# Kernel tuning notes

Measured on AMD Instinct MI355X. Metric: run time of the kernel, lower is better.

The kernel has to match this reference:

```python
import jax, jax.numpy as jnp
import numpy as np
from jax import lax

G, K, C_IN, C_FEAT, H, W, B = 8, 6, 512, 256, 64, 64, 1


def apply_offset(offset):
    # offset: [N, 2, H, W] pixel-space offsets -> sampling grid [N, H, W, 2] in [-1, 1]
    # channel 0 displaces x (width), channel 1 displaces y (height), matching the
    # reversed-meshgrid logic of the original torch apply_offset.
    n, _, h, w = offset.shape
    jj = jnp.arange(w, dtype=offset.dtype)[None, None, :]
    ii = jnp.arange(h, dtype=offset.dtype)[None, :, None]
    gx = (jj + offset[:, 0]) / ((w - 1.0) / 2.0) - 1.0
    gy = (ii + offset[:, 1]) / ((h - 1.0) / 2.0) - 1.0
    return jnp.stack([gx, gy], axis=-1)


def grid_sample_border(img, grid):
    # img: [N, C, H, W], grid: [N, H, W, 2] in [-1, 1]
    # Bilinear, padding_mode='border', align_corners=False (torch grid_sample default).
    n, c, h, w = img.shape
    x = jnp.clip((grid[..., 0] + 1.0) * w * 0.5 - 0.5, 0.0, w - 1.0)
    y = jnp.clip((grid[..., 1] + 1.0) * h * 0.5 - 0.5, 0.0, h - 1.0)
    x0 = jnp.floor(x)
    y0 = jnp.floor(y)
    wx = (x - x0)[:, None]  # [N,1,H,W]
    wy = (y - y0)[:, None]
    x0i = x0.astype(jnp.int32)
    y0i = y0.astype(jnp.int32)
    x1i = jnp.minimum(x0i + 1, w - 1)
    y1i = jnp.minimum(y0i + 1, h - 1)

    def gather(im, yi, xi):  # im [C,H,W]; yi, xi [H,W]
        return im[:, yi, xi]

    g = jax.vmap(gather)
    v00 = g(img, y0i, x0i)
    v01 = g(img, y0i, x1i)
    v10 = g(img, y1i, x0i)
    v11 = g(img, y1i, x1i)
    return (1.0 - wy) * ((1.0 - wx) * v00 + wx * v01) + wy * ((1.0 - wx) * v10 + wx * v11)


def setup_inputs() -> dict:
    key = jax.random.key(0)
    ks = jax.random.split(key, 11)
    s = 0.02
    return {
        "gar_feat": jax.random.normal(ks[0], (B, C_FEAT, H, W), jnp.float32),
        "cond_feat": jax.random.normal(ks[1], (B, C_FEAT, H, W), jnp.float32),
        "mask": jax.random.uniform(ks[2], (B, G, C_FEAT), dtype=jnp.float32),
        "W1": jax.random.normal(ks[3], (G, 128, C_IN, 3, 3), jnp.float32) * s,
        "b1": jax.random.normal(ks[4], (G, 128), jnp.float32) * s,
        "W2": jax.random.normal(ks[5], (G, 64, 128, 3, 3), jnp.float32) * s,
        "b2": jax.random.normal(ks[6], (G, 64), jnp.float32) * s,
        "W3": jax.random.normal(ks[7], (G, 32, 64, 3, 3), jnp.float32) * s,
        "b3": jax.random.normal(ks[8], (G, 32), jnp.float32) * s,
        "W4": jax.random.normal(ks[9], (G, 3 * K, 32, 3, 3), jnp.float32) * s,
        "b4": jax.random.normal(ks[10], (G, 3 * K), jnp.float32) * s,
    }


def reference(gar_feat, cond_feat, mask, W1, b1, W2, b2, W3, b3, W4, b4):
    b, c, h, w = gar_feat.shape
    g = W1.shape[0]
    k = W4.shape[1] // 3
    inp = jnp.concatenate([gar_feat, cond_feat], axis=1)  # [B, 2C, H, W]

    def conv(x, wgt, bias):
        return lax.conv_general_dilated(
            x, wgt, (1, 1), 'SAME', dimension_numbers=('NCHW', 'OIHW', 'NCHW')
        ) + bias[None, :, None, None]

    def lrelu(x):
        return jnp.where(x >= 0, x, 0.1 * x)

    def group_net(w1, bb1, w2, bb2, w3, bb3, w4, bb4):
        hid = lrelu(conv(inp, w1, bb1))
        hid = lrelu(conv(hid, w2, bb2))
        hid = lrelu(conv(hid, w3, bb3))
        return conv(hid, w4, bb4)  # [B, 3k, H, W]

    oa = jax.vmap(group_net)(W1, b1, W2, b2, W3, b3, W4, b4)  # [G, B, 3k, H, W]
    attn = jax.nn.softmax(oa[:, :, 2 * k:], axis=0)           # softmax across groups: [G,B,k,H,W]
    off = oa[:, :, :2 * k].reshape(g, b * k, 2, h, w)
    grid = jax.vmap(apply_offset)(off)                        # [G, B*k, H, W, 2]

    rep = jnp.repeat(gar_feat, k, axis=0)                     # [B*k, C, H, W]

    def warp_group(grid_g, attn_g, mask_g):
        samp = grid_sample_border(rep, grid_g).reshape(b, k, c, h, w)
        wfeat = jnp.sum(samp * attn_g[:, :, None], axis=1)    # [B, C, H, W]
        return wfeat * mask_g[:, :, None, None]

    warped = jax.vmap(warp_group)(grid, attn, jnp.transpose(mask, (1, 0, 2)))
    return jnp.sum(warped, axis=0)  # [B, C, H, W]
```

## Files before the change

kernel.cpp:

```cpp
#include <hip/hip_runtime.h>
#include <hip/hip_bf16.h>

typedef __hip_bfloat16 bf16;
typedef unsigned short ushort8v __attribute__((ext_vector_type(8)));
typedef short  s16x4  __attribute__((ext_vector_type(4)));
typedef short  bf16x8 __attribute__((ext_vector_type(8)));
typedef float  f32x4  __attribute__((ext_vector_type(4)));

#define HW 4096
#define IMG_W 64

__device__ __forceinline__ float bfbits2f(unsigned short u) {
    return __uint_as_float(((unsigned int)u) << 16);
}
__device__ __forceinline__ short f2bs(float f) {
    bf16 h = __float2bfloat16(f);
    return *reinterpret_cast<short*>(&h);
}

__device__ __forceinline__ void gl_lds16(const void* g, void* s) {
    __builtin_amdgcn_global_load_lds(
        (const __attribute__((address_space(1))) unsigned int*)g,
        (__attribute__((address_space(3))) unsigned int*)s, 16, 0, 0);
}

__device__ void pack_input_dev(const float* __restrict__ gar,
                               const float* __restrict__ cond,
                               short* __restrict__ outp,
                               short* __restrict__ gart, int bx2, float* tile)
{
    int bx = bx2 & 127;
    int by = bx2 >> 7;
    int tx = threadIdx.x & 31;
    int ty = threadIdx.x >> 5;
#pragma unroll
    for (int i = 0; i < 4; ++i) {
        int c = by * 32 + ty + i * 8;
        const float* src = (c < 256) ? (gar + (size_t)c * HW)
                                     : (cond + (size_t)(c - 256) * HW);
        tile[(ty + i * 8) * 33 + tx] = src[bx * 32 + tx];
    }
    __syncthreads();
#pragma unroll
    for (int i = 0; i < 4; ++i) {
        int p = bx * 32 + ty + i * 8;
        short v = f2bs(tile[tx * 33 + ty + i * 8]);
        outp[((size_t)by * 4096 + p) * 32 + tx] = v;
        if (by < 8)
            gart[(size_t)p * 256 + by * 32 + tx] = v;
    }
}

template<int CIN, int CREAL, int BN, int NT, bool COAL>
__device__ void pack_w_dev(const float* __restrict__ wgt, char* __restrict__ wp,
                           int bx, short* sT)
{
    constexpr int NCC  = CIN / 32;
    constexpr int BLKB = 9 * 4 * BN * 16;

    const int t  = threadIdx.x;
    const int cc = bx % NCC;
    const int nt = (bx / NCC) % NT;
    const int g  = bx / (NT * NCC);

    for (int i = t; i < BLKB / 8; i += 256)
        reinterpret_cast<s16x4*>(sT)[i] = s16x4{0, 0, 0, 0};
    __syncthreads();

    int ocmax = CREAL - nt * BN; if (ocmax > BN) ocmax = BN;
    const size_t base = ((size_t)(g * CREAL + nt * BN) * CIN + cc * 32) * 9;
    for (int i = t; i < ocmax * 288; i += 256) {
        int oc = i / 288;
        int r  = i % 288;
        int ic = r / 9, tap = r % 9;
        size_t idx;
        if (COAL) idx = (size_t)(((tap * BN + oc) * 4 + (ic >> 3)) * 8 + (ic & 7));
        else      idx = (size_t)(((tap * 4 + (ic >> 3)) * BN + oc) * 8 + (ic & 7));
        sT[idx] = f2bs(wgt[base + (size_t)oc * CIN * 9 + r]);
    }
    __syncthreads();

    const s16x4* src = reinterpret_cast<const s16x4*>(sT);
    s16x4* dst = reinterpret_cast<s16x4*>(wp + (size_t)bx * BLKB);
    for (int i = t; i < BLKB / 8; i += 256)
        dst[i] = src[i];
}

__global__ __launch_bounds__(256)
void pack_all(const float* __restrict__ gar, const float* __restrict__ cond,
              const float* __restrict__ W1, const float* __restrict__ W2,
              const float* __restrict__ W3, const float* __restrict__ W4,
              short* inp_t, short* gar_t,
              char* W1p, char* W2p, char* W3p, char* W4p)
{
    __shared__ __align__(16) short sbuf[9 * 4 * 64 * 8];
    int bx = blockIdx.x;
    if (bx < 256)      pack_w_dev<512, 128, 64, 2, true>(W1, W1p, bx,       sbuf);
    else if (bx < 288) pack_w_dev<128,  64, 64, 1, true>(W2, W2p, bx - 256, sbuf);
    else if (bx < 304) pack_w_dev< 64,  32, 32, 1, true>(W3, W3p, bx - 288, sbuf);
    else if (bx < 312) pack_w_dev< 32,  18, 32, 1, true>(W4, W4p, bx - 304, sbuf);
    else pack_input_dev(gar, cond, inp_t, gar_t, bx - 312, (float*)sbuf);
}

__global__ __launch_bounds__(256, 2)
void conv1_p2(const short* __restrict__ inp, const char* __restrict__ wp,
              const float* __restrict__ bias, short* __restrict__ outp)
{
    __shared__ __align__(16) short sA[2][4][66][4][8];

    const int b  = blockIdx.x;
    const int g  = b & 7;
    const int r_ = b >> 3;
    const int pt = r_ & 31;
    const int nt = r_ >> 5;
    const int r0 = pt * 2;

    const int t    = threadIdx.x;
    const int wave = t >> 6, lane = t & 63;
    const int l15  = lane & 15, quad = lane >> 4;

    const int row_l = wave & 1;
    const int ocw   = (wave >> 1) * 32;

    const short* wb    = (const short*)wp + (size_t)(g * 2 + nt) * 16 * 18432;
    const short* wlane = wb + ((size_t)(ocw + l15) * 4 + quad) * 8;

    auto stageDMA = [&](int cc, int buf) {
        const int gy = r0 - 1 + wave;
        if (gy >= 0 && gy < 64) {
            const short* src = inp + ((size_t)cc * 4096 + (size_t)gy * 64) * 32
                                   + (size_t)lane * 8;
#pragma unroll
            for (int c4 = 0; c4 < 4; ++c4)
                gl_lds16(src + c4 * 512, &sA[buf][wave][1 + c4 * 16][0][0]);
        }
    };

    f32x4 acc[2][4];
#pragma unroll
    for (int o = 0; o < 2; ++o)
#pragma unroll
        for (int f = 0; f < 4; ++f)
#pragma unroll
            for (int r = 0; r < 4; ++r) acc[o][f][r] = 0.f;

    stageDMA(0, 0);
    if (t < 64) {
        int buf = t >> 5, row = (t >> 3) & 3, q = (t >> 1) & 3;
        int col = (t & 1) ? 65 : 0;
        *reinterpret_cast<bf16x8*>(&sA[buf][row][col][q][0]) =
            bf16x8{0, 0, 0, 0, 0, 0, 0, 0};
    }
    if (r0 == 0 || r0 == 62) {
        int zr = (r0 == 0) ? 0 : 3;
        for (int i = t; i < 2 * 66 * 4; i += 256) {
            int buf = i / 264, rem = i % 264;
            *reinterpret_cast<bf16x8*>(&sA[buf][zr][rem >> 2][rem & 3][0]) =
                bf16x8{0, 0, 0, 0, 0, 0, 0, 0};
        }
    }

    bf16x8 w[2][2];
    bf16x8 pf[2][4];
#pragma unroll
    for (int o = 0; o < 2; ++o)
        w[0][o] = *reinterpret_cast<const bf16x8*>(wlane + o * 512);

    auto body = [&](int cc, int cur, int par) {
        const short* wcc = wlane + (size_t)cc * 18432;
        __syncthreads();
        if (cc + 1 < 16) stageDMA(cc + 1, cur ^ 1);
#pragma unroll
        for (int f = 0; f < 4; ++f)
            pf[0][f] = *reinterpret_cast<const bf16x8*>(
                &sA[cur][row_l][f * 16 + l15][quad][0]);
#pragma unroll
        for (int tap = 0; tap < 9; ++tap) {
            const int pb = tap & 1, pn = pb ^ 1;
            const int cb = (tap + par) & 1, nb = cb ^ 1;
            if (tap < 8) {
                const int dy1 = (tap + 1) / 3, dx1 = (tap + 1) % 3;
#pragma unroll
                for (int f = 0; f < 4; ++f)
                    pf[pn][f] = *reinterpret_cast<const bf16x8*>(
                        &sA[cur][row_l + dy1][f * 16 + l15 + dx1][quad][0]);
            }
            const short* nsrc = wcc + (size_t)(tap + 1) * 2048;
#pragma unroll
            for (int o = 0; o < 2; ++o)
                w[nb][o] = *reinterpret_cast<const bf16x8*>(nsrc + o * 512);
            __builtin_amdgcn_sched_barrier(0);
#pragma unroll
            for (int o = 0; o < 2; ++o)
#pragma unroll
                for (int f = 0; f < 4; ++f)
                    acc[o][f] = __builtin_amdgcn_mfma_f32_16x16x32_bf16(
                        w[cb][o], pf[pb][f], acc[o][f], 0, 0, 0);
        }
    };

    for (int c2 = 0; c2 < 16; c2 += 2) {
        body(c2,     0, 0);
        body(c2 + 1, 1, 1);
    }

    const int prow = r0 + row_l;
    const size_t pixbase = (size_t)g * 4096 + (size_t)prow * 64;
#pragma unroll
    for (int o = 0; o < 2; ++o) {
        const int ocb = nt * 64 + ocw + o * 16 + quad * 4;
        const float4 bv4 = *reinterpret_cast<const float4*>(bias + g * 128 + ocb);
        const float bvv[4] = {bv4.x, bv4.y, bv4.z, bv4.w};
#pragma unroll
        for (int f = 0; f < 4; ++f) {
            s16x4 pkt;
#pragma unroll
            for (int reg = 0; reg < 4; ++reg) {
                float v = acc[o][f][reg] + bvv[reg];
                v = v >= 0.f ? v : 0.1f * v;
                pkt[reg] = f2bs(v);
            }
            *reinterpret_cast<s16x4*>(
                outp + (pixbase + f * 16 + l15) * 128 + ocb) = pkt;
        }
    }
}

__global__ __launch_bounds__(512, 2)
void conv2_ss(const short* __restrict__ inp, const char* __restrict__ wp,
              const float* __restrict__ bias, short* __restrict__ outp)
{
    __shared__ __align__(16) short sA[4][4][66][4][8];

    const int b  = blockIdx.x;
    const int g  = b & 7;
    const int pt = b >> 3;
    const int r0 = pt * 2;

    const int t    = threadIdx.x;
    const int wave = t >> 6, lane = t & 63;
    const int l15  = lane & 15, quad = lane >> 4;

    const int row_l = wave & 1;
    const int ocq   = wave >> 1;

    const short* wb    = (const short*)wp + (size_t)g * 4 * 18432;
    const short* wlane = wb + ((size_t)(ocq * 16 + l15) * 4 + quad) * 8;

#pragma unroll
    for (int s = 0; s < 2; ++s) {
        const int u   = wave * 2 + s;
        const int cc  = u >> 2, row = u & 3;
        const int gy  = r0 - 1 + row;
        if (gy >= 0 && gy < 64) {
            const short* rowb = inp + ((size_t)g * 4096 + (size_t)gy * 64) * 128
                                    + cc * 32 + (lane & 3) * 8;
#pragma unroll
            for (int i = 0; i < 4; ++i)
                gl_lds16(rowb + (size_t)(i * 16 + (lane >> 2)) * 128,
                         &sA[cc][row][1 + i * 16][0][0]);
        }
    }
    if (t < 128) {
        int cc = t >> 5, row = (t >> 3) & 3, col = (t & 4) ? 65 : 0, q = t & 3;
        *reinterpret_cast<bf16x8*>(&sA[cc][row][col][q][0]) =
            bf16x8{0, 0, 0, 0, 0, 0, 0, 0};
    }
    if (r0 == 0 || r0 == 62) {
        int zr = (r0 == 0) ? 0 : 3;
        for (int i = t; i < 4 * 264; i += 512) {
            int cc = i / 264, rem = i % 264;
            *reinterpret_cast<bf16x8*>(&sA[cc][zr][rem >> 2][rem & 3][0]) =
                bf16x8{0, 0, 0, 0, 0, 0, 0, 0};
        }
    }

    f32x4 acc[4];
#pragma unroll
    for (int f = 0; f < 4; ++f)
#pragma unroll
        for (int r = 0; r < 4; ++r) acc[f][r] = 0.f;

    bf16x8 w[2];
    bf16x8 pf[2][4];
    w[0] = *reinterpret_cast<const bf16x8*>(wlane);

    __syncthreads();

#pragma unroll
    for (int f = 0; f < 4; ++f)
        pf[0][f] = *reinterpret_cast<const bf16x8*>(
            &sA[0][row_l][f * 16 + l15][quad][0]);

#pragma unroll
    for (int cc = 0; cc < 4; ++cc) {
        const short* wcc = wlane + (size_t)cc * 18432;
#pragma unroll
        for (int tap = 0; tap < 9; ++tap) {
            const int pb = (cc + tap) & 1, pn = pb ^ 1;
            if (tap < 8) {
                const int dy1 = (tap + 1) / 3, dx1 = (tap + 1) % 3;
#pragma unroll
                for (int f = 0; f < 4; ++f)
                    pf[pn][f] = *reinterpret_cast<const bf16x8*>(
                        &sA[cc][row_l + dy1][f * 16 + l15 + dx1][quad][0]);
            } else if (cc < 3) {
#pragma unroll
                for (int f = 0; f < 4; ++f)
                    pf[pn][f] = *reinterpret_cast<const bf16x8*>(
                        &sA[cc + 1][row_l][f * 16 + l15][quad][0]);
            }
            w[pn] = *reinterpret_cast<const bf16x8*>(
                wcc + (size_t)(tap + 1) * 2048);
            __builtin_amdgcn_sched_barrier(0);
#pragma unroll
            for (int f = 0; f < 4; ++f)
                acc[f] = __builtin_amdgcn_mfma_f32_16x16x32_bf16(
                    w[pb], pf[pb][f], acc[f], 0, 0, 0);
        }
    }

    const int prow = r0 + row_l;
    const size_t pixbase = (size_t)g * 4096 + (size_t)prow * 64;
    {
        const int ocb = ocq * 16 + quad * 4;
        const float4 bv4 = *reinterpret_cast<const float4*>(bias + g * 64 + ocb);
        const float bvv[4] = {bv4.x, bv4.y, bv4.z, bv4.w};
#pragma unroll
        for (int f = 0; f < 4; ++f) {
            s16x4 pkt;
#pragma unroll
            for (int reg = 0; reg < 4; ++reg) {
                float v = acc[f][reg] + bvv[reg];
                v = v >= 0.f ? v : 0.1f * v;
                pkt[reg] = f2bs(v);
            }
            *reinterpret_cast<s16x4*>(
                outp + (pixbase + f * 16 + l15) * 64 + ocb) = pkt;
        }
    }
}

__global__ __launch_bounds__(512, 2)
void conv34_p2(const short* __restrict__ hid2, const char* __restrict__ w3p,
               const char* __restrict__ w4p, const float* __restrict__ b3,
               const float* __restrict__ b4, float* __restrict__ oa)
{
    __shared__ __align__(16) short sA[6][2][66][4][8];
    __shared__ __align__(16) short sH3[4][66][4][8];

    const int b  = blockIdx.x;
    const int g  = b & 7;
    const int pt = b >> 3;
    const int r0 = pt * 2;

    const int t    = threadIdx.x;
    const int wave = t >> 6, lane = t & 63;
    const int l15  = lane & 15, quad = lane >> 4;

    const int wrow = wave & 3;
    const int och3 = wave >> 2;
    const int w4row = wave & 1;
    const int och4  = (wave >> 1) & 1;
    const int pxh   = wave >> 2;

    const short* w3lane = (const short*)w3p + (size_t)(g * 2) * 9216
                        + ((size_t)(och3 * 16 + l15) * 4 + quad) * 8;
    const short* w4lane = (const short*)w4p + (size_t)g * 9216
                        + ((size_t)(och4 * 16 + l15) * 4 + quad) * 8;

    if (wave < 6) {
        const int gy = r0 - 2 + wave;
        if (gy >= 0 && gy < 64) {
            const short* src = hid2 + ((size_t)g * 4096 + (size_t)gy * 64) * 64;
#pragma unroll
            for (int cc = 0; cc < 2; ++cc)
#pragma unroll
                for (int i = 0; i < 4; ++i)
                    gl_lds16(src + (size_t)(i * 16 + (lane >> 2)) * 64
                                 + cc * 32 + (lane & 3) * 8,
                             &sA[wave][cc][1 + i * 16][0][0]);
        } else {
            s16x4* rowdst = reinterpret_cast<s16x4*>(&sA[wave][0][0][0][0]);
            for (int i = lane; i < 1056; i += 64)
                rowdst[i] = s16x4{0, 0, 0, 0};
        }
    }
    if (t < 96) {
        int row = t / 16, cc = (t >> 3) & 1, col = (t & 4) ? 65 : 0, q = t & 3;
        *reinterpret_cast<bf16x8*>(&sA[row][cc][col][q][0]) =
            bf16x8{0, 0, 0, 0, 0, 0, 0, 0};
    } else if (t < 128) {
        int i = t - 96;
        int row = i >> 3, col = (i & 4) ? 65 : 0, q = i & 3;
        *reinterpret_cast<bf16x8*>(&sH3[row][col][q][0]) =
            bf16x8{0, 0, 0, 0, 0, 0, 0, 0};
    }

    bf16x8 w[2];
    bf16x8 pf[2][4];
    w[0] = *reinterpret_cast<const bf16x8*>(w3lane);

    f32x4 acc3[4];
#pragma unroll
    for (int f = 0; f < 4; ++f)
#pragma unroll
        for (int r = 0; r < 4; ++r) acc3[f][r] = 0.f;

    __syncthreads();

#pragma unroll
    for (int cc = 0; cc < 2; ++cc) {
        const short* wcc = w3lane + (size_t)cc * 9216;
#pragma unroll
        for (int f = 0; f < 4; ++f)
            pf[0][f] = *reinterpret_cast<const bf16x8*>(
                &sA[wrow][cc][f * 16 + l15][quad][0]);
#pragma unroll
        for (int tap = 0; tap < 9; ++tap) {
            const int pb = tap & 1, pn = pb ^ 1;
            const int cb = (tap + cc) & 1, nb = cb ^ 1;
            if (tap < 8) {
                const int dy1 = (tap + 1) / 3, dx1 = (tap + 1) % 3;
#pragma unroll
                for (int f = 0; f < 4; ++f)
                    pf[pn][f] = *reinterpret_cast<const bf16x8*>(
                        &sA[wrow + dy1][cc][f * 16 + l15 + dx1][quad][0]);
            }
            w[nb] = *reinterpret_cast<const bf16x8*>(
                wcc + (size_t)(tap + 1) * 1024);
            __builtin_amdgcn_sched_barrier(0);
#pragma unroll
            for (int f = 0; f < 4; ++f)
                acc3[f] = __builtin_amdgcn_mfma_f32_16x16x32_bf16(
                    w[cb], pf[pb][f], acc3[f], 0, 0, 0);
        }
    }

    {
        const int gy3 = r0 - 1 + wrow;
        const bool v3 = (gy3 >= 0 && gy3 < 64);
        const int qp = och3 * 2 + (quad >> 1);
        const int e0 = (quad & 1) * 4;
#pragma unroll
        for (int f = 0; f < 4; ++f) {
            s16x4 pkt;
#pragma unroll
            for (int reg = 0; reg < 4; ++reg) {
                const int oc3 = och3 * 16 + quad * 4 + reg;
                float v = acc3[f][reg] + b3[g * 32 + oc3];
                v = v >= 0.f ? v : 0.1f * v;
                pkt[reg] = v3 ? f2bs(v) : (short)0;
            }
            *reinterpret_cast<s16x4*>(&sH3[wrow][1 + f * 16 + l15][qp][e0]) = pkt;
        }
    }
    __syncthreads();

    bf16x8 w4[2];
    bf16x8 pf4[2][2];
    w4[0] = *reinterpret_cast<const bf16x8*>(w4lane);

    f32x4 acc4[2];
#pragma unroll
    for (int f = 0; f < 2; ++f)
#pragma unroll
        for (int r = 0; r < 4; ++r) acc4[f][r] = 0.f;

#pragma unroll
    for (int f = 0; f < 2; ++f)
        pf4[0][f] = *reinterpret_cast<const bf16x8*>(
            &sH3[w4row][pxh * 32 + f * 16 + l15][quad][0]);
#pragma unroll
    for (int tap = 0; tap < 9; ++tap) {
        const int pb = tap & 1, pn = pb ^ 1;
        const int cb = tap & 1, nb = cb ^ 1;
        if (tap < 8) {
            const int dy1 = (tap + 1) / 3, dx1 = (tap + 1) % 3;
#pragma unroll
            for (int f = 0; f < 2; ++f)
                pf4[pn][f] = *reinterpret_cast<const bf16x8*>(
                    &sH3[w4row + dy1][pxh * 32 + f * 16 + l15 + dx1][quad][0]);
        }
        w4[nb] = *reinterpret_cast<const bf16x8*>(
            w4lane + (size_t)(tap + 1) * 1024);
        __builtin_amdgcn_sched_barrier(0);
#pragma unroll
        for (int f = 0; f < 2; ++f)
            acc4[f] = __builtin_amdgcn_mfma_f32_16x16x32_bf16(
                w4[cb], pf4[pb][f], acc4[f], 0, 0, 0);
    }

    const int prow4 = r0 + w4row;
#pragma unroll
    for (int reg = 0; reg < 4; ++reg) {
        const int oc4 = och4 * 16 + quad * 4 + reg;
        if (oc4 < 18) {
            const float bv = b4[g * 18 + oc4];
#pragma unroll
            for (int f = 0; f < 2; ++f)
                oa[(size_t)(g * 18 + oc4) * HW + prow4 * 64 + pxh * 32
                   + f * 16 + l15] = acc4[f][reg] + bv;
        }
    }
}

__global__ __launch_bounds__(256)
void warp_combine_kernel(const float* __restrict__ oa,
                         const short* __restrict__ gar_t,
                         const float* __restrict__ mask,
                         float* __restrict__ out)
{
    __shared__ __align__(16) float4 sWts[8][6][8];
    __shared__ __align__(16) int4   sIdx[8][6][8];

    const int t = threadIdx.x;

    if (t < 48) {
        int lp = t / 6;
        int k  = t % 6;
        int p  = blockIdx.x * 8 + lp;
        int x  = p & 63, y = p >> 6;

        float l[8];
        float m = -1e30f;
#pragma unroll
        for (int g = 0; g < 8; ++g) {
            l[g] = oa[(size_t)(g * 18 + 12 + k) * HW + p];
            m = fmaxf(m, l[g]);
        }
        float s = 0.f;
#pragma unroll
        for (int g = 0; g < 8; ++g) { l[g] = __expf(l[g] - m); s += l[g]; }
        float inv = 1.f / s;

#pragma unroll
        for (int g = 0; g < 8; ++g) {
            float a  = l[g] * inv;
            float ox = oa[(size_t)(g * 18 + 2 * k)     * HW + p];
            float oy = oa[(size_t)(g * 18 + 2 * k + 1) * HW + p];
            float sx = fminf(fmaxf(((float)x + ox) * (64.f / 63.f) - 0.5f, 0.f), 63.f);
            float sy = fminf(fmaxf(((float)y + oy) * (64.f / 63.f) - 0.5f, 0.f), 63.f);
            float fx0 = floorf(sx), fy0 = floorf(sy);
            int   x0 = (int)fx0,    y0i = (int)fy0;
            float wx = sx - fx0,    wy = sy - fy0;
            int   x1 = min(x0 + 1, 63), y1 = min(y0i + 1, 63);
            sWts[lp][k][g] = make_float4(a * (1.f - wy) * (1.f - wx),
                                         a * (1.f - wy) * wx,
                                         a * wy * (1.f - wx),
                                         a * wy * wx);
            sIdx[lp][k][g] = make_int4(y0i * 64 + x0, y0i * 64 + x1,
                                       y1  * 64 + x0, y1  * 64 + x1);
        }
    }
    __syncthreads();

    const int lp = t >> 5;
    const int p  = blockIdx.x * 8 + lp;
    const int c0 = (t & 31) * 8;
    const short* ipc = gar_t + c0;

    float acc[8];
#pragma unroll
    for (int j = 0; j < 8; ++j) acc[j] = 0.f;

    for (int g = 0; g < 8; ++g) {
        float4 m0 = *reinterpret_cast<const float4*>(mask + g * 256 + c0);
        float4 m1 = *reinterpret_cast<const float4*>(mask + g * 256 + c0 + 4);
        float mk[8] = {m0.x, m0.y, m0.z, m0.w, m1.x, m1.y, m1.z, m1.w};
#pragma unroll
        for (int k = 0; k < 6; ++k) {
            float4 w  = sWts[lp][k][g];
            int4   id = sIdx[lp][k][g];
            ushort8v v00 = *reinterpret_cast<const ushort8v*>(ipc + (size_t)id.x * 256);
            ushort8v v01 = *reinterpret_cast<const ushort8v*>(ipc + (size_t)id.y * 256);
            ushort8v v10 = *reinterpret_cast<const ushort8v*>(ipc + (size_t)id.z * 256);
            ushort8v v11 = *reinterpret_cast<const ushort8v*>(ipc + (size_t)id.w * 256);
#pragma unroll
            for (int j = 0; j < 8; ++j) {
                float sv = w.x * bfbits2f(v00[j]) + w.y * bfbits2f(v01[j])
                         + w.z * bfbits2f(v10[j]) + w.w * bfbits2f(v11[j]);
                acc[j] = fmaf(mk[j], sv, acc[j]);
            }
        }
    }
#pragma unroll
    for (int j = 0; j < 8; ++j)
        out[(size_t)(c0 + j) * HW + p] = acc[j];
}

extern "C" void kernel_launch(void* const* d_in, const int* in_sizes, int n_in,
                              void* d_out, int out_size, void* d_ws, size_t ws_size,
                              hipStream_t stream)
{
    (void)in_sizes; (void)n_in; (void)out_size; (void)ws_size;
    const float* gar  = (const float*)d_in[0];
    const float* cond = (const float*)d_in[1];
    const float* mask = (const float*)d_in[2];
    const float* W1   = (const float*)d_in[3];
    const float* b1   = (const float*)d_in[4];
    const float* W2   = (const float*)d_in[5];
    const float* b2   = (const float*)d_in[6];
    const float* W3   = (const float*)d_in[7];
    const float* b3   = (const float*)d_in[8];
    const float* W4   = (const float*)d_in[9];
    const float* b4   = (const float*)d_in[10];
    float* out = (float*)d_out;

    char* ws = (char*)d_ws;
    short* inp_t  = (short*)(ws);
    char*  W1p    = ws + (4u << 20);
    short* hid2_t = (short*)(ws + (4u << 20));
    float* oa     = (float*)(ws + (10u << 20) + (512u << 10));
    char*  W2p    = ws + (14u << 20);
    char*  W3p    = ws + (15u << 20) + (512u << 10);
    char*  W4p    = ws + (16u << 20);
    short* hid1_t = (short*)(ws + (17u << 20));
    short* gar_t  = (short*)(ws + (26u << 20));

    pack_all<<<2360, 256, 0, stream>>>(gar, cond, W1, W2, W3, W4,
                                       inp_t, gar_t, W1p, W2p, W3p, W4p);

    conv1_p2<<<512, 256, 0, stream>>>(inp_t, W1p, b1, hid1_t);
    conv2_ss<<<256, 512, 0, stream>>>(hid1_t, W2p, b2, hid2_t);
    conv34_p2<<<256, 512, 0, stream>>>(hid2_t, W3p, W4p, b3, b4, oa);

    warp_combine_kernel<<<512, 256, 0, stream>>>(oa, gar_t, mask, out);
}
```

Measured before the change: 189.8 us.

## Vectorize packing loads/stores and parallelize softmax prologue across warp lanes

Input packing now uses float4 loads and 4-wide bf16 stores instead of scalar accesses. Weight packing reads float4 weights and copies with 16-byte vectors. The warp-combine prologue spreads the 384 (pixel, k, group) items over all threads and does the softmax across groups with lane shuffles, instead of 48 threads each looping serially. Possible risks are misaligned float4 weight reads, since 288 per oc is divisible by 4, and more LDS bank conflicts in the tile writes.

```diff
diff --git a/kernel.cpp b/kernel.cpp
--- a/kernel.cpp
+++ b/kernel.cpp
@@ -31,23 +31,30 @@
 {
     int bx = bx2 & 127;
     int by = bx2 >> 7;
-    int tx = threadIdx.x & 31;
-    int ty = threadIdx.x >> 5;
-#pragma unroll
-    for (int i = 0; i < 4; ++i) {
-        int c = by * 32 + ty + i * 8;
-        const float* src = (c < 256) ? (gar + (size_t)c * HW)
-                                     : (cond + (size_t)(c - 256) * HW);
-        tile[(ty + i * 8) * 33 + tx] = src[bx * 32 + tx];
+    const int t  = threadIdx.x;
+    const int cg = t >> 3;
+    const int e4 = (t & 7) * 4;
+
+    {
+        int c = by * 32 + cg;
+        const float* src = (by < 8) ? (gar + (size_t)c * HW)
+                                    : (cond + (size_t)(c - 256) * HW);
+        float4 v = *reinterpret_cast<const float4*>(src + bx * 32 + e4);
+        tile[cg * 33 + e4 + 0] = v.x;
+        tile[cg * 33 + e4 + 1] = v.y;
+        tile[cg * 33 + e4 + 2] = v.z;
+        tile[cg * 33 + e4 + 3] = v.w;
     }
     __syncthreads();
-#pragma unroll
-    for (int i = 0; i < 4; ++i) {
-        int p = bx * 32 + ty + i * 8;
-        short v = f2bs(tile[tx * 33 + ty + i * 8]);
-        outp[((size_t)by * 4096 + p) * 32 + tx] = v;
+    {
+        int p = bx * 32 + cg;
+        s16x4 pkt;
+#pragma unroll
+        for (int j = 0; j < 4; ++j)
+            pkt[j] = f2bs(tile[(e4 + j) * 33 + cg]);
+        *reinterpret_cast<s16x4*>(&outp[((size_t)by * 4096 + p) * 32 + e4]) = pkt;
         if (by < 8)
-            gart[(size_t)p * 256 + by * 32 + tx] = v;
+            *reinterpret_cast<s16x4*>(&gart[(size_t)p * 256 + by * 32 + e4]) = pkt;
     }
 }
 
@@ -63,26 +70,33 @@
     const int nt = (bx / NCC) % NT;
     const int g  = bx / (NT * NCC);
 
-    for (int i = t; i < BLKB / 8; i += 256)
-        reinterpret_cast<s16x4*>(sT)[i] = s16x4{0, 0, 0, 0};
+    for (int i = t; i < BLKB / 16; i += 256)
+        reinterpret_cast<bf16x8*>(sT)[i] = bf16x8{0, 0, 0, 0, 0, 0, 0, 0};
     __syncthreads();
 
     int ocmax = CREAL - nt * BN; if (ocmax > BN) ocmax = BN;
     const size_t base = ((size_t)(g * CREAL + nt * BN) * CIN + cc * 32) * 9;
-    for (int i = t; i < ocmax * 288; i += 256) {
-        int oc = i / 288;
-        int r  = i % 288;
-        int ic = r / 9, tap = r % 9;
-        size_t idx;
-        if (COAL) idx = (size_t)(((tap * BN + oc) * 4 + (ic >> 3)) * 8 + (ic & 7));
-        else      idx = (size_t)(((tap * 4 + (ic >> 3)) * BN + oc) * 8 + (ic & 7));
-        sT[idx] = f2bs(wgt[base + (size_t)oc * CIN * 9 + r]);
+    for (int i4 = t * 4; i4 < ocmax * 288; i4 += 1024) {
+        int oc = i4 / 288;
+        int r  = i4 % 288;
+        float4 wv = *reinterpret_cast<const float4*>(
+            &wgt[base + (size_t)oc * CIN * 9 + r]);
+        float wa[4] = {wv.x, wv.y, wv.z, wv.w};
+#pragma unroll
+        for (int j = 0; j < 4; ++j) {
+            int rr = r + j;
+            int ic = rr / 9, tap = rr % 9;
+            size_t idx;
+            if (COAL) idx = (size_t)(((tap * BN + oc) * 4 + (ic >> 3)) * 8 + (ic & 7));
+            else      idx = (size_t)(((tap * 4 + (ic >> 3)) * BN + oc) * 8 + (ic & 7));
+            sT[idx] = f2bs(wa[j]);
+        }
     }
     __syncthreads();
 
-    const s16x4* src = reinterpret_cast<const s16x4*>(sT);
-    s16x4* dst = reinterpret_cast<s16x4*>(wp + (size_t)bx * BLKB);
-    for (int i = t; i < BLKB / 8; i += 256)
+    const bf16x8* src = reinterpret_cast<const bf16x8*>(sT);
+    bf16x8* dst = reinterpret_cast<bf16x8*>(wp + (size_t)bx * BLKB);
+    for (int i = t; i < BLKB / 16; i += 256)
         dst[i] = src[i];
 }
 
@@ -516,43 +530,44 @@
 
     const int t = threadIdx.x;
 
-    if (t < 48) {
-        int lp = t / 6;
-        int k  = t % 6;
-        int p  = blockIdx.x * 8 + lp;
-        int x  = p & 63, y = p >> 6;
-
-        float l[8];
-        float m = -1e30f;
-#pragma unroll
-        for (int g = 0; g < 8; ++g) {
-            l[g] = oa[(size_t)(g * 18 + 12 + k) * HW + p];
-            m = fmaxf(m, l[g]);
-        }
-        float s = 0.f;
-#pragma unroll
-        for (int g = 0; g < 8; ++g) { l[g] = __expf(l[g] - m); s += l[g]; }
-        float inv = 1.f / s;
-
-#pragma unroll
-        for (int g = 0; g < 8; ++g) {
-            float a  = l[g] * inv;
-            float ox = oa[(size_t)(g * 18 + 2 * k)     * HW + p];
-            float oy = oa[(size_t)(g * 18 + 2 * k + 1) * HW + p];
-            float sx = fminf(fmaxf(((float)x + ox) * (64.f / 63.f) - 0.5f, 0.f), 63.f);
-            float sy = fminf(fmaxf(((float)y + oy) * (64.f / 63.f) - 0.5f, 0.f), 63.f);
-            float fx0 = floorf(sx), fy0 = floorf(sy);
-            int   x0 = (int)fx0,    y0i = (int)fy0;
-            float wx = sx - fx0,    wy = sy - fy0;
-            int   x1 = min(x0 + 1, 63), y1 = min(y0i + 1, 63);
-            sWts[lp][k][g] = make_float4(a * (1.f - wy) * (1.f - wx),
-                                         a * (1.f - wy) * wx,
-                                         a * wy * (1.f - wx),
-                                         a * wy * wx);
-            sIdx[lp][k][g] = make_int4(y0i * 64 + x0, y0i * 64 + x1,
-                                       y1  * 64 + x0, y1  * 64 + x1);
-        }
-    }
+    auto do_item = [&](int i) {
+        const int lp  = i / 48;
+        const int rem = i - lp * 48;
+        const int k   = rem >> 3;
+        const int g   = rem & 7;
+        const int p   = blockIdx.x * 8 + lp;
+        const int x   = p & 63, y = p >> 6;
+
+        float lg = oa[(size_t)(g * 18 + 12 + k) * HW + p];
+        float m = lg;
+        m = fmaxf(m, __shfl_xor(m, 1));
+        m = fmaxf(m, __shfl_xor(m, 2));
+        m = fmaxf(m, __shfl_xor(m, 4));
+        float e = __expf(lg - m);
+        float s = e;
+        s += __shfl_xor(s, 1);
+        s += __shfl_xor(s, 2);
+        s += __shfl_xor(s, 4);
+        float a = e / s;
+
+        float ox = oa[(size_t)(g * 18 + 2 * k)     * HW + p];
+        float oy = oa[(size_t)(g * 18 + 2 * k + 1) * HW + p];
+        float sx = fminf(fmaxf(((float)x + ox) * (64.f / 63.f) - 0.5f, 0.f), 63.f);
+        float sy = fminf(fmaxf(((float)y + oy) * (64.f / 63.f) - 0.5f, 0.f), 63.f);
+        float fx0 = floorf(sx), fy0 = floorf(sy);
+        int   x0 = (int)fx0,    y0i = (int)fy0;
+        float wx = sx - fx0,    wy = sy - fy0;
+        int   x1 = min(x0 + 1, 63), y1 = min(y0i + 1, 63);
+        sWts[lp][k][g] = make_float4(a * (1.f - wy) * (1.f - wx),
+                                     a * (1.f - wy) * wx,
+                                     a * wy * (1.f - wx),
+                                     a * wy * wx);
+        sIdx[lp][k][g] = make_int4(y0i * 64 + x0, y0i * 64 + x1,
+                                   y1  * 64 + x0, y1  * 64 + x1);
+    };
+
+    do_item(t);
+    if (t < 128) do_item(256 + t);
     __syncthreads();
 
     const int lp = t >> 5;
```

Result: faster. 180.8 us (-4.7%).
